# Kernel tuning notes

Measured on AMD Instinct MI355X. Metric: run time of the kernel, lower is better.

Reference implementation:

```python
import jax, jax.numpy as jnp
import numpy as np

D = 1024
H = 16
HS = 64

def setup_inputs() -> dict:
    key = jax.random.key(0)
    ks = jax.random.split(key, 9)
    s = 0.02
    x = jax.random.normal(ks[0], (2, 4096, D), dtype=jnp.float32)
    Wq = jax.random.normal(ks[1], (H, D, HS), dtype=jnp.float32) * s
    Wk = jax.random.normal(ks[2], (H, D, HS), dtype=jnp.float32) * s
    Wv = jax.random.normal(ks[3], (H, D, HS), dtype=jnp.float32) * s
    bq = jax.random.normal(ks[4], (H, HS), dtype=jnp.float32) * s
    bk = jax.random.normal(ks[5], (H, HS), dtype=jnp.float32) * s
    bv = jax.random.normal(ks[6], (H, HS), dtype=jnp.float32) * s
    Wp = jax.random.normal(ks[7], (D, D), dtype=jnp.float32) * s
    bp = jax.random.normal(ks[8], (D,), dtype=jnp.float32) * s
    return {"x": x, "Wq": Wq, "Wk": Wk, "Wv": Wv, "bq": bq, "bk": bk, "bv": bv, "Wp": Wp, "bp": bp}

def reference(x, Wq, Wk, Wv, bq, bk, bv, Wp, bp):
    B, T, _ = x.shape
    # per-head projections, stacked over heads: [B, H, T, HS]
    q = jnp.einsum('btd,hde->bhte', x, Wq) + bq[None, :, None, :]
    k = jnp.einsum('btd,hde->bhte', x, Wk) + bk[None, :, None, :]
    v = jnp.einsum('btd,hde->bhte', x, Wv) + bv[None, :, None, :]
    scale = 1.0 / jnp.sqrt(jnp.float32(HS))
    scores = jnp.einsum('bhte,bhse->bhts', q, k) * scale  # [B,H,T,T]
    causal = jnp.tril(jnp.ones((T, T), dtype=bool))
    scores = jnp.where(causal[None, None, :, :], scores, -jnp.inf)
    attn = jax.nn.softmax(scores, axis=-1)
    out = jnp.einsum('bhts,bhse->bhte', attn, v)  # [B,H,T,HS]
    # concat heads along last dim (head order preserved)
    out = out.transpose(0, 2, 1, 3).reshape(B, T, H * HS)
    return out @ Wp + bp
```

## Files before the change

kernel.cpp:

```cpp
#include <hip/hip_runtime.h>
#include <hip/hip_bf16.h>
#include <stdint.h>


typedef __bf16 bf16x8 __attribute__((ext_vector_type(8)));
typedef unsigned short ushort8v __attribute__((ext_vector_type(8)));
typedef float f32x4 __attribute__((ext_vector_type(4)));
typedef float f32x16 __attribute__((ext_vector_type(16)));
typedef __attribute__((address_space(1))) void gvoid_t;
typedef __attribute__((address_space(3))) void lvoid_t;

using hbf = __hip_bfloat16;

#define QSCALE (0.125f * 1.44269504088896f)

static __device__ __forceinline__ void gload_lds16(const void* g, void* l) {
  __builtin_amdgcn_global_load_lds((gvoid_t*)g, (lvoid_t*)l, 16, 0, 0);
}

static __device__ __forceinline__ uint16_t b2u(float x) {
  hbf h = __float2bfloat16(x);
  return *reinterpret_cast<uint16_t*>(&h);
}

static __device__ __forceinline__ uint32_t cvtpk(float lo, float hi) {
  uint32_t r;
  asm("v_cvt_pk_bf16_f32 %0, %1, %2" : "=v"(r) : "v"(lo), "v"(hi));
  return r;
}

static __device__ __forceinline__ void pl32swap(uint32_t& x, uint32_t& y) {
  asm volatile("v_permlane32_swap_b32 %0, %1" : "+v"(x), "+v"(y));
}

static __device__ __forceinline__ float max3f(float a, float b, float c) {
  return fmaxf(fmaxf(a, b), c);
}


__global__ void k_cvt_x_bias(const float* __restrict__ x,
                             const float* __restrict__ bq, const float* __restrict__ bk,
                             const float* __restrict__ bv,
                             hbf* __restrict__ xb, float* __restrict__ biasc) {
  const int b = blockIdx.x, tid = threadIdx.x;
  if (b < 8192) {
    int i = (b * 256 + tid) * 4;
    float4 v = *reinterpret_cast<const float4*>(x + i);
    hbf h[4] = {__float2bfloat16(v.x), __float2bfloat16(v.y),
                __float2bfloat16(v.z), __float2bfloat16(v.w)};
    *reinterpret_cast<ushort4*>(xb + i) = *reinterpret_cast<ushort4*>(h);
  } else {
    int r = (b - 8192) * 256 + tid;
    int m = r >> 10, rem = r & 1023;
    const float* bsrc = (m == 0) ? bq : (m == 1) ? bk : bv;
    float v = bsrc[rem];
    if (m == 0) v *= QSCALE;
    biasc[r] = v;
  }
}

__global__ void k_cvt_wqkv(const float* __restrict__ Wq, const float* __restrict__ Wk,
                           const float* __restrict__ Wv, hbf* __restrict__ Wt) {
  __shared__ float lds[64][65];
  const int b = blockIdx.x, tid = threadIdx.x;
  const int m = b >> 8, h = (b >> 4) & 15, d0 = (b & 15) * 64;
  const float* W = (m == 0) ? Wq : (m == 1) ? Wk : Wv;

  const int dr = tid >> 4, ec = (tid & 15) * 4;
#pragma unroll
  for (int p = 0; p < 4; ++p) {
    const int row = p * 16 + dr;
    float4 v = *reinterpret_cast<const float4*>(
        W + ((size_t)((h << 10) + d0 + row)) * 64 + ec);
    if (m == 0) { v.x *= QSCALE; v.y *= QSCALE; v.z *= QSCALE; v.w *= QSCALE; }
    lds[row][ec] = v.x; lds[row][ec + 1] = v.y;
    lds[row][ec + 2] = v.z; lds[row][ec + 3] = v.w;
  }
  __syncthreads();

  const int e = tid >> 2, dj = (tid & 3) * 16;
  uint16_t tmp[16];
#pragma unroll
  for (int j = 0; j < 16; ++j) tmp[j] = b2u(lds[dj + j][e]);
  hbf* dst = Wt + ((size_t)(m * 1024 + (h << 6) + e)) * 1024 + d0 + dj;
  *reinterpret_cast<ushort8v*>(dst) = *reinterpret_cast<ushort8v*>(tmp);
  *reinterpret_cast<ushort8v*>(dst + 8) = *reinterpret_cast<ushort8v*>(tmp + 8);
}

__global__ void k_cvt_wp(const float* __restrict__ Wp, hbf* __restrict__ Wpt) {
  __shared__ float lds[64][65];
  const int b = blockIdx.x, tid = threadIdx.x;
  const int d0 = (b >> 4) * 64, o0 = (b & 15) * 64;

  const int dr = tid >> 4, oc = (tid & 15) * 4;
#pragma unroll
  for (int p = 0; p < 4; ++p) {
    const int row = p * 16 + dr;
    float4 v = *reinterpret_cast<const float4*>(Wp + (size_t)(d0 + row) * 1024 + o0 + oc);
    lds[row][oc] = v.x; lds[row][oc + 1] = v.y;
    lds[row][oc + 2] = v.z; lds[row][oc + 3] = v.w;
  }
  __syncthreads();

  const int ol = tid >> 2, dj = (tid & 3) * 16;
  uint16_t tmp[16];
#pragma unroll
  for (int j = 0; j < 16; ++j) tmp[j] = b2u(lds[dj + j][ol]);
  hbf* dst = Wpt + (size_t)(o0 + ol) * 1024 + d0 + dj;
  *reinterpret_cast<ushort8v*>(dst) = *reinterpret_cast<ushort8v*>(tmp);
  *reinterpret_cast<ushort8v*>(dst + 8) = *reinterpret_cast<ushort8v*>(tmp + 8);
}


__global__ __launch_bounds__(512) void k_gemm_qkv(
    const hbf* __restrict__ A, const hbf* __restrict__ Bw,
    const float* __restrict__ biasc, hbf* __restrict__ qkv) {
  __shared__ __align__(16) hbf sA[2][128 * 64];
  __shared__ __align__(16) hbf sB[2][256 * 64];
  const int tid = threadIdx.x;
  const int lane = tid & 63, w = tid >> 6;
  const int wm = w >> 2, wn = w & 3;
  const int g = lane >> 4, cl = lane & 15;
  const int m0 = blockIdx.x * 128, n0 = blockIdx.y * 256;
  const int sr = tid >> 3, sc = tid & 7;

  const f32x4 fz = {0.f, 0.f, 0.f, 0.f};
  f32x4 acc[4][4];
#pragma unroll
  for (int a = 0; a < 4; ++a)
#pragma unroll
    for (int b = 0; b < 4; ++b) acc[a][b] = fz;

#pragma unroll
  for (int kt = 0; kt < 2; ++kt) {
#pragma unroll
    for (int s = 0; s < 2; ++s) {
      const int row = s * 64 + sr;
      gload_lds16(A + (size_t)(m0 + row) * 1024 + kt * 64 + ((sc ^ (row & 7)) * 8),
                  &sA[kt][s * 4096 + tid * 8]);
    }
#pragma unroll
    for (int s = 0; s < 4; ++s) {
      const int row = s * 64 + sr;
      gload_lds16(Bw + (size_t)(n0 + row) * 1024 + kt * 64 + ((sc ^ (row & 7)) * 8),
                  &sB[kt][s * 4096 + tid * 8]);
    }
  }
  asm volatile("s_waitcnt vmcnt(6)" ::: "memory");
  __builtin_amdgcn_s_barrier();

  for (int kt = 0; kt < 16; ++kt) {
    const int bi = kt & 1;
    const bool st = (kt + 2) < 16;

    bf16x8 af[4][2], bf[4][2];
#pragma unroll
    for (int rt = 0; rt < 4; ++rt)
#pragma unroll
      for (int ks = 0; ks < 2; ++ks)
        af[rt][ks] = *reinterpret_cast<const bf16x8*>(
            &sA[bi][(wm * 64 + rt * 16 + cl) * 64 + (((ks * 4 + g) ^ (cl & 7)) * 8)]);
#pragma unroll
    for (int ct = 0; ct < 4; ++ct)
#pragma unroll
      for (int ks = 0; ks < 2; ++ks)
        bf[ct][ks] = *reinterpret_cast<const bf16x8*>(
            &sB[bi][(wn * 64 + ct * 16 + cl) * 64 + (((ks * 4 + g) ^ (cl & 7)) * 8)]);
    __builtin_amdgcn_s_barrier();
    asm volatile("s_waitcnt lgkmcnt(0)" ::: "memory");
    __builtin_amdgcn_sched_barrier(0);
    __builtin_amdgcn_s_setprio(1);
#pragma unroll
    for (int rt = 0; rt < 4; ++rt)
#pragma unroll
      for (int ks = 0; ks < 2; ++ks)
        acc[rt][0] = __builtin_amdgcn_mfma_f32_16x16x32_bf16(af[rt][ks], bf[0][ks], acc[rt][0], 0, 0, 0);
    __builtin_amdgcn_s_setprio(0);
    __builtin_amdgcn_s_barrier();

#pragma unroll
    for (int q = 1; q < 4; ++q) {
      if (st) {
        if (q == 1) {
#pragma unroll
          for (int s = 0; s < 2; ++s) {
            const int row = s * 64 + sr;
            gload_lds16(A + (size_t)(m0 + row) * 1024 + (kt + 2) * 64 + ((sc ^ (row & 7)) * 8),
                        &sA[bi][s * 4096 + tid * 8]);
          }
        } else {
#pragma unroll
          for (int s2 = 0; s2 < 2; ++s2) {
            const int s = (q - 2) * 2 + s2;
            const int row = s * 64 + sr;
            gload_lds16(Bw + (size_t)(n0 + row) * 1024 + (kt + 2) * 64 + ((sc ^ (row & 7)) * 8),
                        &sB[bi][s * 4096 + tid * 8]);
          }
        }
      }
      __builtin_amdgcn_s_setprio(1);
#pragma unroll
      for (int rt = 0; rt < 4; ++rt)
#pragma unroll
        for (int ks = 0; ks < 2; ++ks)
          acc[rt][q] = __builtin_amdgcn_mfma_f32_16x16x32_bf16(af[rt][ks], bf[q][ks], acc[rt][q], 0, 0, 0);
      __builtin_amdgcn_s_setprio(0);
      if (q == 3) {
        if (st) asm volatile("s_waitcnt vmcnt(6)" ::: "memory");
        else    asm volatile("s_waitcnt vmcnt(0)" ::: "memory");
      }
      __builtin_amdgcn_s_barrier();
    }
  }

#pragma unroll
  for (int rt = 0; rt < 4; ++rt)
#pragma unroll
    for (int ct = 0; ct < 4; ++ct) {
      const int colg = n0 + wn * 64 + ct * 16 + cl;
      const int mi = colg >> 10, rem = colg & 1023;
      const int h = rem >> 6, e = rem & 63;
      const float bi_ = biasc[colg];
      if (mi == 2) {
        const int t0 = m0 + wm * 64 + rt * 16 + g * 4;
        const int b = t0 >> 12, t = t0 & 4095;
        ushort4 o;
        o.x = b2u(acc[rt][ct][0] + bi_);
        o.y = b2u(acc[rt][ct][1] + bi_);
        o.z = b2u(acc[rt][ct][2] + bi_);
        o.w = b2u(acc[rt][ct][3] + bi_);
        *reinterpret_cast<ushort4*>(
            qkv + (size_t)64 * 262144 + (size_t)(b * 16 + h) * 262144 + (size_t)e * 4096 + t) = o;
      } else {
#pragma unroll
        for (int i = 0; i < 4; ++i) {
          const int rowg = m0 + wm * 64 + rt * 16 + g * 4 + i;
          const int b = rowg >> 12, t = rowg & 4095;
          qkv[(((size_t)mi * 32 + b * 16 + h) * 4096 + t) * 64 + e] =
              __float2bfloat16(acc[rt][ct][i] + bi_);
        }
      }
    }
}


__global__ __launch_bounds__(512) void k_flash(
    const hbf* __restrict__ qkv, hbf* __restrict__ attn) {
  __shared__ __align__(16) __bf16 sK[2][64 * 64];
  __shared__ __align__(16) __bf16 sV[2][64 * 64];
  const int tid = threadIdx.x, lane = tid & 63, wq = tid >> 6;
  const int h = lane >> 5, r31 = lane & 31;
  const int bh = blockIdx.x;
  const int y = (int)blockIdx.y;
  const int qtb = (y < 8) ? (15 - y) : (y - 8);
  const int q0 = qtb * 256;
  const int ntile = 4 * qtb + 4;
  const hbf* Q  = qkv + (size_t)bh * 262144;
  const hbf* Kp = qkv + (size_t)(32 + bh) * 262144;
  const hbf* Vp = qkv + (size_t)(64 + bh) * 262144;
  const float NEG_INF = -__builtin_inff();

  const int sr = tid >> 3, sc = tid & 7;
  const int koff = sr * 64 + ((sc ^ (sr & 7)) * 8);
  const int voff = sr * 4096 + ((sc ^ (sr & 7)) * 8);

  const int qrow = q0 + wq * 32 + r31;
  bf16x8 aq[4];
#pragma unroll
  for (int ks = 0; ks < 4; ++ks)
    aq[ks] = *reinterpret_cast<const bf16x8*>(Q + (size_t)qrow * 64 + ks * 16 + h * 8);

  f32x16 accO[2];
#pragma unroll
  for (int et = 0; et < 2; ++et)
#pragma unroll
    for (int i = 0; i < 16; ++i) accO[et][i] = 0.f;
  float mrow = NEG_INF, lrow = 0.f;

  gload_lds16(Kp + koff, &sK[0][tid * 8]);
  gload_lds16(Vp + voff, &sV[0][tid * 8]);
  __syncthreads();

  const int qmaxw = q0 + wq * 32 + 31;
  int buf = 0;
  for (int jt = 0; jt < ntile; ++jt) {
    if (jt < ntile - 1) {
      gload_lds16(Kp + (size_t)(jt + 1) * 4096 + koff, &sK[buf ^ 1][tid * 8]);
      gload_lds16(Vp + (jt + 1) * 64 + voff,           &sV[buf ^ 1][tid * 8]);
    }

    if (64 * jt <= qmaxw) {
      const __bf16* sKb = sK[buf];
      const __bf16* sVb = sV[buf];

      f32x16 accS[2];
      __builtin_amdgcn_s_setprio(1);
#pragma unroll
      for (int t = 0; t < 2; ++t) {
        f32x16 s;
#pragma unroll
        for (int i = 0; i < 16; ++i) s[i] = 0.f;
#pragma unroll
        for (int ks = 0; ks < 4; ++ks) {
          bf16x8 ak = *reinterpret_cast<const bf16x8*>(
              sKb + (t * 32 + r31) * 64 + (((2 * ks + h) ^ (r31 & 7)) * 8));
          s = __builtin_amdgcn_mfma_f32_32x32x16_bf16(ak, aq[ks], s, 0, 0, 0);
        }
        accS[t] = s;
      }
      __builtin_amdgcn_s_setprio(0);

      if (64 * jt + 63 > q0 + wq * 32) {
#pragma unroll
        for (int t = 0; t < 2; ++t)
#pragma unroll
          for (int i = 0; i < 16; ++i) {
            const int kvg = 64 * jt + 32 * t + (i & 3) + 8 * (i >> 2) + 4 * h;
            if (kvg > qrow) accS[t][i] = NEG_INF;
          }
      }

      float g0 = max3f(accS[0][0], accS[0][1], accS[0][2]);
      float g1 = max3f(accS[0][3], accS[0][4], accS[0][5]);
      float g2 = max3f(accS[0][6], accS[0][7], accS[0][8]);
      float g3 = max3f(accS[0][9], accS[0][10], accS[0][11]);
      float g4 = max3f(accS[0][12], accS[0][13], accS[0][14]);
      float g5 = max3f(accS[0][15], accS[1][0], accS[1][1]);
      float g6 = max3f(accS[1][2], accS[1][3], accS[1][4]);
      float g7 = max3f(accS[1][5], accS[1][6], accS[1][7]);
      float g8 = max3f(accS[1][8], accS[1][9], accS[1][10]);
      float g9 = max3f(accS[1][11], accS[1][12], accS[1][13]);
      float gA = fmaxf(accS[1][14], accS[1][15]);
      float h0 = max3f(g0, g1, g2);
      float h1 = max3f(g3, g4, g5);
      float h2 = max3f(g6, g7, g8);
      float h3 = fmaxf(g9, gA);
      float pmax = fmaxf(max3f(h0, h1, h2), h3);
      pmax = fmaxf(pmax, __shfl_xor(pmax, 32));

      if (!__all(pmax - mrow <= 8.f)) {
        const float mn = fmaxf(mrow, pmax);
        const float corr = __builtin_amdgcn_exp2f(mrow - mn);
        mrow = mn;
        lrow *= corr;
#pragma unroll
        for (int et = 0; et < 2; ++et)
#pragma unroll
          for (int i = 0; i < 16; ++i) accO[et][i] *= corr;
      }

#pragma unroll
      for (int t = 0; t < 2; ++t)
#pragma unroll
        for (int i = 0; i < 16; ++i)
          accS[t][i] = __builtin_amdgcn_exp2f(accS[t][i] - mrow);
      float s0 = (accS[0][0] + accS[0][1]) + (accS[0][2] + accS[0][3]);
      float s1 = (accS[0][4] + accS[0][5]) + (accS[0][6] + accS[0][7]);
      float s2 = (accS[0][8] + accS[0][9]) + (accS[0][10] + accS[0][11]);
      float s3 = (accS[0][12] + accS[0][13]) + (accS[0][14] + accS[0][15]);
      float s4 = (accS[1][0] + accS[1][1]) + (accS[1][2] + accS[1][3]);
      float s5 = (accS[1][4] + accS[1][5]) + (accS[1][6] + accS[1][7]);
      float s6 = (accS[1][8] + accS[1][9]) + (accS[1][10] + accS[1][11]);
      float s7 = (accS[1][12] + accS[1][13]) + (accS[1][14] + accS[1][15]);
      float rs = ((s0 + s1) + (s2 + s3)) + ((s4 + s5) + (s6 + s7));
      rs += __shfl_xor(rs, 32);
      lrow += rs;

      uint32_t d0[2][4], d1[2][4];
#pragma unroll
      for (int t = 0; t < 2; ++t)
#pragma unroll
        for (int r4 = 0; r4 < 4; ++r4) {
          d0[t][r4] = cvtpk(accS[t][4 * r4 + 0], accS[t][4 * r4 + 1]);
          d1[t][r4] = cvtpk(accS[t][4 * r4 + 2], accS[t][4 * r4 + 3]);
        }

#pragma unroll
      for (int kb = 0; kb < 4; ++kb) {
        const int t = kb >> 1, ra = 2 * (kb & 1), rb = ra + 1;
        uint32_t x0 = d0[t][ra], y0 = d0[t][rb];
        uint32_t x1 = d1[t][ra], y1 = d1[t][rb];
        pl32swap(x0, y0);
        pl32swap(x1, y1);
        union { uint32_t u[4]; bf16x8 v; } bP;
        bP.u[0] = x0; bP.u[1] = x1; bP.u[2] = y0; bP.u[3] = y1;
        __builtin_amdgcn_s_setprio(1);
#pragma unroll
        for (int et = 0; et < 2; ++et) {
          bf16x8 av = *reinterpret_cast<const bf16x8*>(
              sVb + (et * 32 + r31) * 64 + (((2 * kb + h) ^ (r31 & 7)) * 8));
          accO[et] = __builtin_amdgcn_mfma_f32_32x32x16_bf16(av, bP.v, accO[et], 0, 0, 0);
        }
        __builtin_amdgcn_s_setprio(0);
      }
    }

    __syncthreads();
    buf ^= 1;
  }

  const float inv = 1.0f / lrow;
  hbf* arow = attn + ((size_t)(bh >> 4) * 4096 + qrow) * 1024 + (bh & 15) * 64;
#pragma unroll
  for (int et = 0; et < 2; ++et)
#pragma unroll
    for (int r4 = 0; r4 < 4; ++r4) {
      const int e0 = et * 32 + 8 * r4 + 4 * h;
      ushort4 o;
      o.x = b2u(accO[et][4 * r4 + 0] * inv);
      o.y = b2u(accO[et][4 * r4 + 1] * inv);
      o.z = b2u(accO[et][4 * r4 + 2] * inv);
      o.w = b2u(accO[et][4 * r4 + 3] * inv);
      *reinterpret_cast<ushort4*>(arow + e0) = o;
    }
}


__global__ __launch_bounds__(512) void k_gemm_out(
    const hbf* __restrict__ A, const hbf* __restrict__ Bw,
    const float* __restrict__ bp, float* __restrict__ out) {
  __shared__ __align__(16) hbf sA[2][128 * 64];
  __shared__ __align__(16) hbf sB[2][256 * 64];
  const int tid = threadIdx.x;
  const int lane = tid & 63, w = tid >> 6;
  const int wm = w >> 2, wn = w & 3;
  const int g = lane >> 4, cl = lane & 15;
  const int m0 = blockIdx.x * 128, n0 = blockIdx.y * 256;
  const int sr = tid >> 3, sc = tid & 7;

  const f32x4 fz = {0.f, 0.f, 0.f, 0.f};
  f32x4 acc[4][4];
#pragma unroll
  for (int a = 0; a < 4; ++a)
#pragma unroll
    for (int b = 0; b < 4; ++b) acc[a][b] = fz;

#pragma unroll
  for (int kt = 0; kt < 2; ++kt) {
#pragma unroll
    for (int s = 0; s < 2; ++s) {
      const int row = s * 64 + sr;
      gload_lds16(A + (size_t)(m0 + row) * 1024 + kt * 64 + ((sc ^ (row & 7)) * 8),
                  &sA[kt][s * 4096 + tid * 8]);
    }
#pragma unroll
    for (int s = 0; s < 4; ++s) {
      const int row = s * 64 + sr;
      gload_lds16(Bw + (size_t)(n0 + row) * 1024 + kt * 64 + ((sc ^ (row & 7)) * 8),
                  &sB[kt][s * 4096 + tid * 8]);
    }
  }
  asm volatile("s_waitcnt vmcnt(6)" ::: "memory");
  __builtin_amdgcn_s_barrier();

  for (int kt = 0; kt < 16; ++kt) {
    const int bi = kt & 1;
    const bool st = (kt + 2) < 16;

    bf16x8 af[4][2], bf[4][2];
#pragma unroll
    for (int rt = 0; rt < 4; ++rt)
#pragma unroll
      for (int ks = 0; ks < 2; ++ks)
        af[rt][ks] = *reinterpret_cast<const bf16x8*>(
            &sA[bi][(wm * 64 + rt * 16 + cl) * 64 + (((ks * 4 + g) ^ (cl & 7)) * 8)]);
#pragma unroll
    for (int ct = 0; ct < 4; ++ct)
#pragma unroll
      for (int ks = 0; ks < 2; ++ks)
        bf[ct][ks] = *reinterpret_cast<const bf16x8*>(
            &sB[bi][(wn * 64 + ct * 16 + cl) * 64 + (((ks * 4 + g) ^ (cl & 7)) * 8)]);
    __builtin_amdgcn_s_barrier();
    asm volatile("s_waitcnt lgkmcnt(0)" ::: "memory");
    __builtin_amdgcn_sched_barrier(0);
    __builtin_amdgcn_s_setprio(1);
#pragma unroll
    for (int rt = 0; rt < 4; ++rt)
#pragma unroll
      for (int ks = 0; ks < 2; ++ks)
        acc[rt][0] = __builtin_amdgcn_mfma_f32_16x16x32_bf16(af[rt][ks], bf[0][ks], acc[rt][0], 0, 0, 0);
    __builtin_amdgcn_s_setprio(0);
    __builtin_amdgcn_s_barrier();

#pragma unroll
    for (int q = 1; q < 4; ++q) {
      if (st) {
        if (q == 1) {
#pragma unroll
          for (int s = 0; s < 2; ++s) {
            const int row = s * 64 + sr;
            gload_lds16(A + (size_t)(m0 + row) * 1024 + (kt + 2) * 64 + ((sc ^ (row & 7)) * 8),
                        &sA[bi][s * 4096 + tid * 8]);
          }
        } else {
#pragma unroll
          for (int s2 = 0; s2 < 2; ++s2) {
            const int s = (q - 2) * 2 + s2;
            const int row = s * 64 + sr;
            gload_lds16(Bw + (size_t)(n0 + row) * 1024 + (kt + 2) * 64 + ((sc ^ (row & 7)) * 8),
                        &sB[bi][s * 4096 + tid * 8]);
          }
        }
      }
      __builtin_amdgcn_s_setprio(1);
#pragma unroll
      for (int rt = 0; rt < 4; ++rt)
#pragma unroll
        for (int ks = 0; ks < 2; ++ks)
          acc[rt][q] = __builtin_amdgcn_mfma_f32_16x16x32_bf16(af[rt][ks], bf[q][ks], acc[rt][q], 0, 0, 0);
      __builtin_amdgcn_s_setprio(0);
      if (q == 3) {
        if (st) asm volatile("s_waitcnt vmcnt(6)" ::: "memory");
        else    asm volatile("s_waitcnt vmcnt(0)" ::: "memory");
      }
      __builtin_amdgcn_s_barrier();
    }
  }

#pragma unroll
  for (int rt = 0; rt < 4; ++rt)
#pragma unroll
    for (int ct = 0; ct < 4; ++ct) {
      const int colg = n0 + wn * 64 + ct * 16 + cl;
      const float bi_ = bp[colg];
#pragma unroll
      for (int i = 0; i < 4; ++i) {
        const int rowg = m0 + wm * 64 + rt * 16 + g * 4 + i;
        out[(size_t)rowg * 1024 + colg] = acc[rt][ct][i] + bi_;
      }
    }
}


extern "C" void kernel_launch(void* const* d_in, const int* in_sizes, int n_in,
                              void* d_out, int out_size, void* d_ws, size_t ws_size,
                              hipStream_t stream) {
  const float* x  = (const float*)d_in[0];
  const float* Wq = (const float*)d_in[1];
  const float* Wk = (const float*)d_in[2];
  const float* Wv = (const float*)d_in[3];
  const float* bq = (const float*)d_in[4];
  const float* bk = (const float*)d_in[5];
  const float* bv = (const float*)d_in[6];
  const float* Wp = (const float*)d_in[7];
  const float* bp = (const float*)d_in[8];
  float* out = (float*)d_out;

  char* ws = (char*)d_ws;
  hbf*   xb    = (hbf*)ws;
  hbf*   Wt    = (hbf*)(ws + 16777216);
  hbf*   Wpt   = (hbf*)(ws + 16777216 + 6291456);
  float* biasc = (float*)(ws + 16777216 + 6291456 + 2097152);
  hbf*   qkv   = (hbf*)(ws + 16777216 + 6291456 + 2097152 + 16384);
  hbf*   attn  = xb;

  k_cvt_x_bias<<<8204, 256, 0, stream>>>(x, bq, bk, bv, xb, biasc);
  k_cvt_wqkv  <<<768,  256, 0, stream>>>(Wq, Wk, Wv, Wt);
  k_cvt_wp    <<<256,  256, 0, stream>>>(Wp, Wpt);

  dim3 g1(64, 12); k_gemm_qkv<<<g1, 512, 0, stream>>>(xb, Wt, biasc, qkv);
  dim3 g2(32, 16); k_flash   <<<g2, 512, 0, stream>>>(qkv, attn);
  dim3 g3(64, 4);  k_gemm_out<<<g3, 512, 0, stream>>>(attn, Wpt, bp, out);
}
```

Before: 198.9 us.

## Merge conversion kernels and process two KV tiles per flash-attention barrier

Folds the three fp32-to-bf16 conversion kernels into one launch, removing two kernel launches and their gaps. In the flash kernel, K/V shared-memory staging grows from two to four buffers and the loop handles two 64-key tiles per iteration, prefetching the next two tiles at once. This halves the number of block-wide barriers and lets each load batch arrive earlier. In exchange it doubles the flash kernel's shared-memory footprint, which may reduce occupancy. The conversion kernel now allocates LDS in every block, including the many elementwise x blocks that never use it.

```diff
diff --git a/kernel.cpp b/kernel.cpp
--- a/kernel.cpp
+++ b/kernel.cpp
@@ -38,10 +38,15 @@
 }
 
 
-__global__ void k_cvt_x_bias(const float* __restrict__ x,
-                             const float* __restrict__ bq, const float* __restrict__ bk,
-                             const float* __restrict__ bv,
-                             hbf* __restrict__ xb, float* __restrict__ biasc) {
+__global__ void k_cvt_all(const float* __restrict__ x,
+                          const float* __restrict__ Wq, const float* __restrict__ Wk,
+                          const float* __restrict__ Wv,
+                          const float* __restrict__ bq, const float* __restrict__ bk,
+                          const float* __restrict__ bv,
+                          const float* __restrict__ Wp,
+                          hbf* __restrict__ xb, hbf* __restrict__ Wt,
+                          hbf* __restrict__ Wpt, float* __restrict__ biasc) {
+  __shared__ float lds[64][65];
   const int b = blockIdx.x, tid = threadIdx.x;
   if (b < 8192) {
     int i = (b * 256 + tid) * 4;
@@ -49,66 +54,55 @@
     hbf h[4] = {__float2bfloat16(v.x), __float2bfloat16(v.y),
                 __float2bfloat16(v.z), __float2bfloat16(v.w)};
     *reinterpret_cast<ushort4*>(xb + i) = *reinterpret_cast<ushort4*>(h);
-  } else {
+  } else if (b < 8204) {
     int r = (b - 8192) * 256 + tid;
     int m = r >> 10, rem = r & 1023;
     const float* bsrc = (m == 0) ? bq : (m == 1) ? bk : bv;
     float v = bsrc[rem];
     if (m == 0) v *= QSCALE;
     biasc[r] = v;
+  } else if (b < 8972) {
+    const int bb = b - 8204;
+    const int m = bb >> 8, h = (bb >> 4) & 15, d0 = (bb & 15) * 64;
+    const float* W = (m == 0) ? Wq : (m == 1) ? Wk : Wv;
+    const int dr = tid >> 4, ec = (tid & 15) * 4;
+#pragma unroll
+    for (int p = 0; p < 4; ++p) {
+      const int row = p * 16 + dr;
+      float4 v = *reinterpret_cast<const float4*>(
+          W + ((size_t)((h << 10) + d0 + row)) * 64 + ec);
+      if (m == 0) { v.x *= QSCALE; v.y *= QSCALE; v.z *= QSCALE; v.w *= QSCALE; }
+      lds[row][ec] = v.x; lds[row][ec + 1] = v.y;
+      lds[row][ec + 2] = v.z; lds[row][ec + 3] = v.w;
+    }
+    __syncthreads();
+    const int e = tid >> 2, dj = (tid & 3) * 16;
+    uint16_t tmp[16];
+#pragma unroll
+    for (int j = 0; j < 16; ++j) tmp[j] = b2u(lds[dj + j][e]);
+    hbf* dst = Wt + ((size_t)(m * 1024 + (h << 6) + e)) * 1024 + d0 + dj;
+    *reinterpret_cast<ushort8v*>(dst) = *reinterpret_cast<ushort8v*>(tmp);
+    *reinterpret_cast<ushort8v*>(dst + 8) = *reinterpret_cast<ushort8v*>(tmp + 8);
+  } else {
+    const int bb = b - 8972;
+    const int d0 = (bb >> 4) * 64, o0 = (bb & 15) * 64;
+    const int dr = tid >> 4, oc = (tid & 15) * 4;
+#pragma unroll
+    for (int p = 0; p < 4; ++p) {
+      const int row = p * 16 + dr;
+      float4 v = *reinterpret_cast<const float4*>(Wp + (size_t)(d0 + row) * 1024 + o0 + oc);
+      lds[row][oc] = v.x; lds[row][oc + 1] = v.y;
+      lds[row][oc + 2] = v.z; lds[row][oc + 3] = v.w;
+    }
+    __syncthreads();
+    const int ol = tid >> 2, dj = (tid & 3) * 16;
+    uint16_t tmp[16];
+#pragma unroll
+    for (int j = 0; j < 16; ++j) tmp[j] = b2u(lds[dj + j][ol]);
+    hbf* dst = Wpt + (size_t)(o0 + ol) * 1024 + d0 + dj;
+    *reinterpret_cast<ushort8v*>(dst) = *reinterpret_cast<ushort8v*>(tmp);
+    *reinterpret_cast<ushort8v*>(dst + 8) = *reinterpret_cast<ushort8v*>(tmp + 8);
   }
-}
-
-__global__ void k_cvt_wqkv(const float* __restrict__ Wq, const float* __restrict__ Wk,
-                           const float* __restrict__ Wv, hbf* __restrict__ Wt) {
-  __shared__ float lds[64][65];
-  const int b = blockIdx.x, tid = threadIdx.x;
-  const int m = b >> 8, h = (b >> 4) & 15, d0 = (b & 15) * 64;
-  const float* W = (m == 0) ? Wq : (m == 1) ? Wk : Wv;
-
-  const int dr = tid >> 4, ec = (tid & 15) * 4;
-#pragma unroll
-  for (int p = 0; p < 4; ++p) {
-    const int row = p * 16 + dr;
-    float4 v = *reinterpret_cast<const float4*>(
-        W + ((size_t)((h << 10) + d0 + row)) * 64 + ec);
-    if (m == 0) { v.x *= QSCALE; v.y *= QSCALE; v.z *= QSCALE; v.w *= QSCALE; }
-    lds[row][ec] = v.x; lds[row][ec + 1] = v.y;
-    lds[row][ec + 2] = v.z; lds[row][ec + 3] = v.w;
-  }
-  __syncthreads();
-
-  const int e = tid >> 2, dj = (tid & 3) * 16;
-  uint16_t tmp[16];
-#pragma unroll
-  for (int j = 0; j < 16; ++j) tmp[j] = b2u(lds[dj + j][e]);
-  hbf* dst = Wt + ((size_t)(m * 1024 + (h << 6) + e)) * 1024 + d0 + dj;
-  *reinterpret_cast<ushort8v*>(dst) = *reinterpret_cast<ushort8v*>(tmp);
-  *reinterpret_cast<ushort8v*>(dst + 8) = *reinterpret_cast<ushort8v*>(tmp + 8);
-}
-
-__global__ void k_cvt_wp(const float* __restrict__ Wp, hbf* __restrict__ Wpt) {
-  __shared__ float lds[64][65];
-  const int b = blockIdx.x, tid = threadIdx.x;
-  const int d0 = (b >> 4) * 64, o0 = (b & 15) * 64;
-
-  const int dr = tid >> 4, oc = (tid & 15) * 4;
-#pragma unroll
-  for (int p = 0; p < 4; ++p) {
-    const int row = p * 16 + dr;
-    float4 v = *reinterpret_cast<const float4*>(Wp + (size_t)(d0 + row) * 1024 + o0 + oc);
-    lds[row][oc] = v.x; lds[row][oc + 1] = v.y;
-    lds[row][oc + 2] = v.z; lds[row][oc + 3] = v.w;
-  }
-  __syncthreads();
-
-  const int ol = tid >> 2, dj = (tid & 3) * 16;
-  uint16_t tmp[16];
-#pragma unroll
-  for (int j = 0; j < 16; ++j) tmp[j] = b2u(lds[dj + j][ol]);
-  hbf* dst = Wpt + (size_t)(o0 + ol) * 1024 + d0 + dj;
-  *reinterpret_cast<ushort8v*>(dst) = *reinterpret_cast<ushort8v*>(tmp);
-  *reinterpret_cast<ushort8v*>(dst + 8) = *reinterpret_cast<ushort8v*>(tmp + 8);
 }
 
 
@@ -246,8 +240,8 @@
 
 __global__ __launch_bounds__(512) void k_flash(
     const hbf* __restrict__ qkv, hbf* __restrict__ attn) {
-  __shared__ __align__(16) __bf16 sK[2][64 * 64];
-  __shared__ __align__(16) __bf16 sV[2][64 * 64];
+  __shared__ __align__(16) __bf16 sK[4][64 * 64];
+  __shared__ __align__(16) __bf16 sV[4][64 * 64];
   const int tid = threadIdx.x, lane = tid & 63, wq = tid >> 6;
   const int h = lane >> 5, r31 = lane & 31;
   const int bh = blockIdx.x;
@@ -277,36 +271,44 @@
     for (int i = 0; i < 16; ++i) accO[et][i] = 0.f;
   float mrow = NEG_INF, lrow = 0.f;
 
-  gload_lds16(Kp + koff, &sK[0][tid * 8]);
-  gload_lds16(Vp + voff, &sV[0][tid * 8]);
+  gload_lds16(Kp + koff,        &sK[0][tid * 8]);
+  gload_lds16(Vp + voff,        &sV[0][tid * 8]);
+  gload_lds16(Kp + 4096 + koff, &sK[1][tid * 8]);
+  gload_lds16(Vp + 64 + voff,   &sV[1][tid * 8]);
   __syncthreads();
 
   const int qmaxw = q0 + wq * 32 + 31;
-  int buf = 0;
-  for (int jt = 0; jt < ntile; ++jt) {
-    if (jt < ntile - 1) {
-      gload_lds16(Kp + (size_t)(jt + 1) * 4096 + koff, &sK[buf ^ 1][tid * 8]);
-      gload_lds16(Vp + (jt + 1) * 64 + voff,           &sV[buf ^ 1][tid * 8]);
-    }
-
-    if (64 * jt <= qmaxw) {
-      const __bf16* sKb = sK[buf];
-      const __bf16* sVb = sV[buf];
+  const int nsuper = ntile >> 1;
+  for (int s = 0; s < nsuper; ++s) {
+    const int jt0 = 2 * s;
+    if (jt0 + 2 < ntile) {
+      gload_lds16(Kp + (size_t)(jt0 + 2) * 4096 + koff, &sK[(jt0 + 2) & 3][tid * 8]);
+      gload_lds16(Vp + (jt0 + 2) * 64 + voff,           &sV[(jt0 + 2) & 3][tid * 8]);
+      gload_lds16(Kp + (size_t)(jt0 + 3) * 4096 + koff, &sK[(jt0 + 3) & 3][tid * 8]);
+      gload_lds16(Vp + (jt0 + 3) * 64 + voff,           &sV[(jt0 + 3) & 3][tid * 8]);
+    }
+
+#pragma unroll
+    for (int sub = 0; sub < 2; ++sub) {
+      const int jt = jt0 + sub;
+      if (64 * jt > qmaxw) break;
+      const __bf16* sKb = sK[jt & 3];
+      const __bf16* sVb = sV[jt & 3];
 
       f32x16 accS[2];
       __builtin_amdgcn_s_setprio(1);
 #pragma unroll
       for (int t = 0; t < 2; ++t) {
-        f32x16 s;
-#pragma unroll
-        for (int i = 0; i < 16; ++i) s[i] = 0.f;
+        f32x16 sacc;
+#pragma unroll
+        for (int i = 0; i < 16; ++i) sacc[i] = 0.f;
 #pragma unroll
         for (int ks = 0; ks < 4; ++ks) {
           bf16x8 ak = *reinterpret_cast<const bf16x8*>(
               sKb + (t * 32 + r31) * 64 + (((2 * ks + h) ^ (r31 & 7)) * 8));
-          s = __builtin_amdgcn_mfma_f32_32x32x16_bf16(ak, aq[ks], s, 0, 0, 0);
+          sacc = __builtin_amdgcn_mfma_f32_32x32x16_bf16(ak, aq[ks], sacc, 0, 0, 0);
         }
-        accS[t] = s;
+        accS[t] = sacc;
       }
       __builtin_amdgcn_s_setprio(0);
 
@@ -396,7 +398,6 @@
     }
 
     __syncthreads();
-    buf ^= 1;
   }
 
   const float inv = 1.0f / lrow;
@@ -554,9 +555,8 @@
   hbf*   qkv   = (hbf*)(ws + 16777216 + 6291456 + 2097152 + 16384);
   hbf*   attn  = xb;
 
-  k_cvt_x_bias<<<8204, 256, 0, stream>>>(x, bq, bk, bv, xb, biasc);
-  k_cvt_wqkv  <<<768,  256, 0, stream>>>(Wq, Wk, Wv, Wt);
-  k_cvt_wp    <<<256,  256, 0, stream>>>(Wp, Wpt);
+  k_cvt_all<<<9228, 256, 0, stream>>>(x, Wq, Wk, Wv, bq, bk, bv, Wp,
+                                      xb, Wt, Wpt, biasc);
 
   dim3 g1(64, 12); k_gemm_qkv<<<g1, 512, 0, stream>>>(xb, Wt, biasc, qkv);
   dim3 g2(32, 16); k_flash   <<<g2, 512, 0, stream>>>(qkv, attn);
```

New measurement: 198.4 us. Within noise of the previous version (-0.3%).
